# Performance work log

Hardware: AMD Instinct MI355X
Metric: run time of the kernel (lower is better)

Reference implementation:

```python
import jax, jax.numpy as jnp
import numpy as np

H = 8
D = 64
SCALER = 1.0 / np.sqrt(D).astype(np.float32)


def setup_inputs() -> dict:
    key = jax.random.key(0)
    k1, k2 = jax.random.split(key)
    B, N, C = 2, 256, 512
    x = jax.random.normal(k1, (B, N, C), dtype=jnp.float32)
    # Linear(C, 5C, bias=False): weight shape [5C, C], torch convention y = x @ W.T
    w = jax.random.normal(k2, (5 * C, C), dtype=jnp.float32) * 0.02
    return {"x": x, "w": w}


def reference(x, w):
    B, N, C = x.shape
    # projections: a, b, c, vj, vk each [B, H, N, D]
    wx = (x @ w.T).reshape(B, N, 5, H, D).transpose(2, 0, 3, 1, 4)
    a, b, c, vj, vk = wx[0], wx[1], wx[2], wx[3], wx[4]

    # three pairwise score matrices, each [B, H, N, N]
    X = jnp.einsum('bhjd,bhkd->bhjk', b, c) * SCALER
    Y = jnp.einsum('bhkd,bhid->bhki', c, a) * SCALER
    Z = jnp.einsum('bhid,bhjd->bhij', a, b) * SCALER

    # custom 3-way softmax stabilization: X uses global max over (j,k),
    # Y uses max over k (axis -2), Z uses max over j (axis -1)
    X = jnp.exp(X - jnp.max(X, axis=(-2, -1), keepdims=True))
    Y = jnp.exp(Y - jnp.max(Y, axis=-2, keepdims=True))
    Z = jnp.exp(Z - jnp.max(Z, axis=-1, keepdims=True))

    # Num_{bhid} = sum_{j,k} Z_ij * X_jk * vj_jd * Y_ki * vk_kd
    # (same math as the original 5D 'bhjkd'/'bhikd' chain, fused via einsum path)
    Num = jnp.einsum('bhij,bhjk,bhjd,bhki,bhkd->bhid', Z, X, vj, Y, vk)
    # Den_{bhi} = sum_{j,k} Z_ij * Y_ki * X_jk
    Den = jnp.einsum('bhij,bhki,bhjk->bhi', Z, Y, X) + 1e-9

    att = Num / Den[..., None]                     # [B, H, N, D]
    att = att.transpose(0, 2, 1, 3).reshape(B, N, C)
    return att
```

## Files before the change

kernel.cpp:

```cpp
#include <hip/hip_runtime.h>
#include <math.h>

#define Bn 2
#define Hn 8
#define Nn 256
#define Dn 64
#define BH 16
#define SCALER 0.125f

typedef _Float16 half8 __attribute__((ext_vector_type(8)));
typedef _Float16 half4 __attribute__((ext_vector_type(4)));
typedef float floatx4 __attribute__((ext_vector_type(4)));

__device__ __forceinline__ void split_f32(float v, _Float16& h, _Float16& l) {
    h = (_Float16)v;
    l = (_Float16)(v - (float)h);
}

__device__ __forceinline__ void split8(const float4& v0, const float4& v1,
                                       half8& h, half8& l) {
    const float vv[8] = {v0.x, v0.y, v0.z, v0.w, v1.x, v1.y, v1.z, v1.w};
    #pragma unroll
    for (int e = 0; e < 8; ++e) {
        _Float16 hh, ll;
        split_f32(vv[e], hh, ll);
        h[e] = hh; l[e] = ll;
    }
}

__global__ __launch_bounds__(256) void split2_kernel(
    const float* __restrict__ x, const float* __restrict__ w,
    _Float16* __restrict__ xh, _Float16* __restrict__ xl,
    _Float16* __restrict__ wh, _Float16* __restrict__ wl) {
    const int b = blockIdx.x;
    const float* src;
    _Float16 *hp, *lp;
    int idx;
    if (b < 256) {
        idx = (b * 256 + threadIdx.x) * 4;
        src = x; hp = xh; lp = xl;
    } else {
        idx = ((b - 256) * 256 + threadIdx.x) * 4;
        src = w; hp = wh; lp = wl;
    }
    const float4 v = *(const float4*)(src + idx);
    half4 hh, ll;
    _Float16 a2, b2;
    split_f32(v.x, a2, b2); hh[0] = a2; ll[0] = b2;
    split_f32(v.y, a2, b2); hh[1] = a2; ll[1] = b2;
    split_f32(v.z, a2, b2); hh[2] = a2; ll[2] = b2;
    split_f32(v.w, a2, b2); hh[3] = a2; ll[3] = b2;
    *(half4*)(hp + idx) = hh;
    *(half4*)(lp + idx) = ll;
}

__global__ __launch_bounds__(256) void proj_mfma(
    const _Float16* __restrict__ xh, const _Float16* __restrict__ xl,
    const _Float16* __restrict__ wh, const _Float16* __restrict__ wl,
    float* __restrict__ P32, float* __restrict__ vkT) {
    const int m0 = blockIdx.x * 64;
    const int r0 = blockIdx.y * 64;
    const int t = threadIdx.x;
    const int w = t >> 6, l = t & 63;
    const int lr = l & 15, kk8 = (l >> 4) * 8;

    floatx4 acc[4];
    #pragma unroll
    for (int ni = 0; ni < 4; ++ni) acc[ni] = (floatx4){0.f, 0.f, 0.f, 0.f};

    const int arow = m0 + w * 16 + lr;
    for (int kt = 0; kt < 16; ++kt) {
        const int k0 = kt * 32 + kk8;
        const half8 ah = *(const half8*)(xh + arow * 512 + k0);
        const half8 al = *(const half8*)(xl + arow * 512 + k0);
        half8 bhv[4], blv[4];
        #pragma unroll
        for (int ni = 0; ni < 4; ++ni) {
            const int wr = r0 + ni * 16 + lr;
            bhv[ni] = *(const half8*)(wh + wr * 512 + k0);
            blv[ni] = *(const half8*)(wl + wr * 512 + k0);
        }
        #pragma unroll
        for (int ni = 0; ni < 4; ++ni)
            acc[ni] = __builtin_amdgcn_mfma_f32_16x16x32_f16(ah, bhv[ni], acc[ni], 0, 0, 0);
        #pragma unroll
        for (int ni = 0; ni < 4; ++ni)
            acc[ni] = __builtin_amdgcn_mfma_f32_16x16x32_f16(ah, blv[ni], acc[ni], 0, 0, 0);
        #pragma unroll
        for (int ni = 0; ni < 4; ++ni)
            acc[ni] = __builtin_amdgcn_mfma_f32_16x16x32_f16(al, bhv[ni], acc[ni], 0, 0, 0);
    }
    const int rbase = (l >> 4) * 4;
    if (blockIdx.y >= 32) {
        const int mbase = m0 + w * 16 + rbase;
        const int b = mbase >> 8, n = mbase & 255;
        #pragma unroll
        for (int ni = 0; ni < 4; ++ni) {
            const int rcol = r0 + ni * 16 + lr;
            const int h = (rcol >> 6) & 7, d = rcol & 63;
            *(float4*)(vkT + (((b * 8 + h) * 64 + d) * 256 + n)) =
                (float4){acc[ni][0], acc[ni][1], acc[ni][2], acc[ni][3]};
        }
        return;
    }
    #pragma unroll
    for (int ni = 0; ni < 4; ++ni) {
        const int rcol = r0 + ni * 16 + lr;
        const int s = rcol >> 9, h = (rcol >> 6) & 7, d = rcol & 63;
        #pragma unroll
        for (int r = 0; r < 4; ++r) {
            const int m = m0 + w * 16 + rbase + r;
            const int b = m >> 8, n = m & 255;
            P32[(((s * 2 + b) * 8 + h) * 256 + n) * 64 + d] = acc[ni][r];
        }
    }
}

__global__ __launch_bounds__(256) void score_vkt(
    const float* __restrict__ P32,
    _Float16* __restrict__ Xsh, _Float16* __restrict__ Xsl,
    float* __restrict__ Yt, float* __restrict__ Z) {
    const int bh = blockIdx.x, mat = blockIdx.y;
    const int t = threadIdx.x;
    const int i0 = (blockIdx.z >> 2) * 128;
    const int j0 = (blockIdx.z & 3) * 64;
    const int w = t >> 6, l = t & 63;
    const int lr = l & 15, kk8 = (l >> 4) * 8;
    const float* A;
    const float* Bm;
    if (mat == 0)      { A = P32 + (1 * 16 + bh) * 16384; Bm = P32 + (2 * 16 + bh) * 16384; }
    else if (mat == 1) { A = P32 + (0 * 16 + bh) * 16384; Bm = P32 + (2 * 16 + bh) * 16384; }
    else               { A = P32 + (0 * 16 + bh) * 16384; Bm = P32 + (1 * 16 + bh) * 16384; }

    floatx4 acc[2][4];
    #pragma unroll
    for (int mi = 0; mi < 2; ++mi)
        #pragma unroll
        for (int ni = 0; ni < 4; ++ni) acc[mi][ni] = (floatx4){0.f, 0.f, 0.f, 0.f};

    for (int kt = 0; kt < 2; ++kt) {
        const int k0 = kt * 32 + kk8;
        half8 ah[2], al[2], bh8[4], bl8[4];
        #pragma unroll
        for (int mi = 0; mi < 2; ++mi) {
            const int row = i0 + w * 32 + mi * 16 + lr;
            const float4 v0 = *(const float4*)(A + row * 64 + k0);
            const float4 v1 = *(const float4*)(A + row * 64 + k0 + 4);
            split8(v0, v1, ah[mi], al[mi]);
        }
        #pragma unroll
        for (int ni = 0; ni < 4; ++ni) {
            const int row = j0 + ni * 16 + lr;
            const float4 v0 = *(const float4*)(Bm + row * 64 + k0);
            const float4 v1 = *(const float4*)(Bm + row * 64 + k0 + 4);
            split8(v0, v1, bh8[ni], bl8[ni]);
        }
        #pragma unroll
        for (int mi = 0; mi < 2; ++mi)
            #pragma unroll
            for (int ni = 0; ni < 4; ++ni)
                acc[mi][ni] = __builtin_amdgcn_mfma_f32_16x16x32_f16(ah[mi], bh8[ni], acc[mi][ni], 0, 0, 0);
        #pragma unroll
        for (int mi = 0; mi < 2; ++mi)
            #pragma unroll
            for (int ni = 0; ni < 4; ++ni)
                acc[mi][ni] = __builtin_amdgcn_mfma_f32_16x16x32_f16(ah[mi], bl8[ni], acc[mi][ni], 0, 0, 0);
        #pragma unroll
        for (int mi = 0; mi < 2; ++mi)
            #pragma unroll
            for (int ni = 0; ni < 4; ++ni)
                acc[mi][ni] = __builtin_amdgcn_mfma_f32_16x16x32_f16(al[mi], bh8[ni], acc[mi][ni], 0, 0, 0);
    }
    const int rbase = (l >> 4) * 4;
    #pragma unroll
    for (int mi = 0; mi < 2; ++mi)
        #pragma unroll
        for (int ni = 0; ni < 4; ++ni)
            #pragma unroll
            for (int r = 0; r < 4; ++r) {
                const int row = i0 + w * 32 + mi * 16 + rbase + r;
                const int col = j0 + ni * 16 + lr;
                const float e = expf(acc[mi][ni][r] * SCALER);
                if (mat == 0) {
                    const int idx = (bh * 256 + row) * 256 + col;
                    _Float16 hh, ll; split_f32(e, hh, ll);
                    Xsh[idx] = hh; Xsl[idx] = ll;
                } else if (mat == 1) {
                    Yt[bh * 65536 + row * 256 + col] = e;
                } else {
                    Z[bh * 65536 + row * 256 + col] = e;
                }
            }
}

__global__ __launch_bounds__(256) void den_mfma(
    const float* __restrict__ Yt, const _Float16* __restrict__ Xh,
    const _Float16* __restrict__ Xl, const float* __restrict__ Z,
    float* __restrict__ Den) {
    const int bh = blockIdx.x;
    const int ibase = blockIdx.y * 16;
    const int t = threadIdx.x;
    const int w = t >> 6, l = t & 63;
    const int lr = l & 15, ks = l >> 4, kk8 = ks * 8;
    const float* Ytp = Yt + bh * 65536;
    const _Float16* Xhp = Xh + bh * 65536;
    const _Float16* Xlp = Xl + bh * 65536;

    floatx4 acc[4];
    #pragma unroll
    for (int q = 0; q < 4; ++q) acc[q] = (floatx4){0.f, 0.f, 0.f, 0.f};

    for (int kt = 0; kt < 8; ++kt) {
        const int k0 = kt * 32 + kk8;
        half8 ah, al;
        {
            const float4 v0 = *(const float4*)(Ytp + (ibase + lr) * 256 + k0);
            const float4 v1 = *(const float4*)(Ytp + (ibase + lr) * 256 + k0 + 4);
            split8(v0, v1, ah, al);
        }
        half8 bh8[4], bl8[4];
        #pragma unroll
        for (int q = 0; q < 4; ++q) {
            const int jt = w * 4 + q;
            bh8[q] = *(const half8*)(Xhp + (jt * 16 + lr) * 256 + k0);
            bl8[q] = *(const half8*)(Xlp + (jt * 16 + lr) * 256 + k0);
        }
        #pragma unroll
        for (int q = 0; q < 4; ++q)
            acc[q] = __builtin_amdgcn_mfma_f32_16x16x32_f16(ah, bh8[q], acc[q], 0, 0, 0);
        #pragma unroll
        for (int q = 0; q < 4; ++q)
            acc[q] = __builtin_amdgcn_mfma_f32_16x16x32_f16(ah, bl8[q], acc[q], 0, 0, 0);
        #pragma unroll
        for (int q = 0; q < 4; ++q)
            acc[q] = __builtin_amdgcn_mfma_f32_16x16x32_f16(al, bh8[q], acc[q], 0, 0, 0);
    }
    __shared__ float redS[4][16];
    float dp[4] = {0.f, 0.f, 0.f, 0.f};
    const float* Zp = Z + (bh * 256 + ibase) * 256;
    #pragma unroll
    for (int q = 0; q < 4; ++q) {
        const int jt = w * 4 + q;
        #pragma unroll
        for (int r = 0; r < 4; ++r)
            dp[r] += acc[q][r] * Zp[(ks * 4 + r) * 256 + jt * 16 + lr];
    }
    #pragma unroll
    for (int r = 0; r < 4; ++r) {
        float s = dp[r];
        s += __shfl_xor(s, 1); s += __shfl_xor(s, 2);
        s += __shfl_xor(s, 4); s += __shfl_xor(s, 8);
        if (lr == 0) redS[w][ks * 4 + r] = s;
    }
    __syncthreads();
    if (t < 16)
        Den[bh * 256 + ibase + t] =
            redS[0][t] + redS[1][t] + redS[2][t] + redS[3][t] + 1e-9f;
}

__global__ __launch_bounds__(256, 2) void attn_mfma(
    const _Float16* __restrict__ Xh, const _Float16* __restrict__ Xl,
    const float* __restrict__ Yt, const float* __restrict__ Z,
    const float* __restrict__ vkT, const float* __restrict__ P32,
    const float* __restrict__ Den, float* __restrict__ out) {
    const int id = (blockIdx.x & 7) * 256 + (blockIdx.x >> 3);
    const int bh = id >> 7;
    const int i0 = (id & 127) * 2;
    const int t = threadIdx.x;
    const int w = t >> 6, l = t & 63;
    const int lr = l & 15, ks = l >> 4, kk8 = ks * 8;

    __shared__ float yiS[2][256], ziS[2][256];
    __shared__ _Float16 BhS[2][2][4096], BlS[2][2][4096];
    float (*redN)[2][64] = reinterpret_cast<float (*)[2][64]>(&yiS[0][0]);

    yiS[0][t] = Yt[(bh * 256 + i0) * 256 + t];
    yiS[1][t] = Yt[(bh * 256 + i0 + 1) * 256 + t];
    ziS[0][t] = Z[(bh * 256 + i0) * 256 + t];
    ziS[1][t] = Z[(bh * 256 + i0 + 1) * 256 + t];

    const _Float16* Xhp = Xh + bh * 65536;
    const _Float16* Xlp = Xl + bh * 65536;
    const float* vkp = vkT + bh * 16384;
    const float* vj = P32 + (3 * 16 + bh) * 16384;

    floatx4 acc[4][8];
    #pragma unroll
    for (int mi = 0; mi < 4; ++mi)
        #pragma unroll
        for (int ct = 0; ct < 8; ++ct) acc[mi][ct] = (floatx4){0.f, 0.f, 0.f, 0.f};

    const int vd = t >> 2;
    const int sl = t & 3;
    float4 vkr[4];

    auto VKLOAD = [&](int kt) {
        const float* gp = vkp + vd * 256 + (kt & 3) * 64 + sl * 16;
        #pragma unroll
        for (int q = 0; q < 4; ++q) vkr[q] = *(const float4*)(gp + q * 4);
    };
    auto BSTORE = [&](int ktb) {
        const int buf = ktb & 1;
        #pragma unroll
        for (int i = 0; i < 2; ++i) {
            const float* yrow = &yiS[i][(ktb & 3) * 64 + sl * 16];
            #pragma unroll
            for (int hq = 0; hq < 2; ++hq) {
                const float4 va = vkr[hq * 2], vb = vkr[hq * 2 + 1];
                const float4 ya = *(const float4*)(yrow + hq * 8);
                const float4 yb = *(const float4*)(yrow + hq * 8 + 4);
                const float pv[8] = {va.x * ya.x, va.y * ya.y, va.z * ya.z, va.w * ya.w,
                                     vb.x * yb.x, vb.y * yb.y, vb.z * yb.z, vb.w * yb.w};
                half8 hv, lv;
                #pragma unroll
                for (int e = 0; e < 8; ++e) {
                    _Float16 hh, ll;
                    split_f32(pv[e], hh, ll);
                    hv[e] = hh; lv[e] = ll;
                }
                const int o = sl * 2 + hq;
                const int g = vd * 8 + (o ^ (vd & 7));
                *(half8*)&BhS[buf][i][g * 8] = hv;
                *(half8*)&BlS[buf][i][g * 8] = lv;
            }
        }
    };
    auto LOADA = [&](half8* AH, half8* AL, int kt, int sub) {
        const int k0 = (kt & 3) * 64 + sub * 32 + kk8;
        #pragma unroll
        for (int mi = 0; mi < 4; ++mi) {
            const int row = w * 64 + mi * 16 + lr;
            AH[mi] = *(const half8*)(Xhp + row * 256 + k0);
            AL[mi] = *(const half8*)(Xlp + row * 256 + k0);
        }
    };
    auto MFMA_STEP = [&](half8* AH, half8* AL, int buf, int sub) {
        __builtin_amdgcn_s_setprio(1);
        #pragma unroll
        for (int ct = 0; ct < 8; ++ct) {
            const int ii = ct >> 2;
            const int dd = (ct & 3) * 16 + lr;
            const int o = sub * 4 + ks;
            const int g = dd * 8 + (o ^ (dd & 7));
            const half8 bhf = *(const half8*)&BhS[buf][ii][g * 8];
            const half8 blf = *(const half8*)&BlS[buf][ii][g * 8];
            #pragma unroll
            for (int mi = 0; mi < 4; ++mi)
                acc[mi][ct] = __builtin_amdgcn_mfma_f32_16x16x32_f16(AH[mi], bhf, acc[mi][ct], 0, 0, 0);
            #pragma unroll
            for (int mi = 0; mi < 4; ++mi)
                acc[mi][ct] = __builtin_amdgcn_mfma_f32_16x16x32_f16(AH[mi], blf, acc[mi][ct], 0, 0, 0);
            #pragma unroll
            for (int mi = 0; mi < 4; ++mi)
                acc[mi][ct] = __builtin_amdgcn_mfma_f32_16x16x32_f16(AL[mi], bhf, acc[mi][ct], 0, 0, 0);
        }
        __builtin_amdgcn_s_setprio(0);
    };

    half8 A0h[4], A0l[4], A1h[4], A1l[4];

    VKLOAD(0);
    LOADA(A0h, A0l, 0, 0);
    __syncthreads();
    BSTORE(0);
    __syncthreads();

    #pragma unroll 1
    for (int kt = 0; kt < 4; ++kt) {
        const int buf = kt & 1;
        if (kt < 3) VKLOAD(kt + 1);
        LOADA(A1h, A1l, kt, 1);
        MFMA_STEP(A0h, A0l, buf, 0);
        if (kt < 3) {
            asm volatile("s_waitcnt vmcnt(8)" ::: "memory");
            __builtin_amdgcn_sched_barrier(0);
            BSTORE(kt + 1);
            LOADA(A0h, A0l, kt + 1, 0);
        }
        MFMA_STEP(A1h, A1l, buf, 1);
        if (kt < 3) __syncthreads();
    }

    float z0[16], z1[16];
    #pragma unroll
    for (int mi = 0; mi < 4; ++mi)
        #pragma unroll
        for (int r = 0; r < 4; ++r) {
            const int j = w * 64 + mi * 16 + ks * 4 + r;
            z0[mi * 4 + r] = ziS[0][j];
            z1[mi * 4 + r] = ziS[1][j];
        }
    #pragma unroll
    for (int dt = 0; dt < 4; ++dt) {
        float n0 = 0.f, n1 = 0.f;
        #pragma unroll
        for (int mi = 0; mi < 4; ++mi)
            #pragma unroll
            for (int r = 0; r < 4; ++r) {
                const int j = w * 64 + mi * 16 + ks * 4 + r;
                const float v = vj[j * 64 + dt * 16 + lr];
                n0 += acc[mi][dt][r] * z0[mi * 4 + r] * v;
                n1 += acc[mi][dt + 4][r] * z1[mi * 4 + r] * v;
            }
        n0 += __shfl_xor(n0, 16); n0 += __shfl_xor(n0, 32);
        n1 += __shfl_xor(n1, 16); n1 += __shfl_xor(n1, 32);
        if (l < 16) {
            redN[w][0][dt * 16 + l] = n0;
            redN[w][1][dt * 16 + l] = n1;
        }
    }
    __syncthreads();
    if (t < 128) {
        const int ih = t >> 6, d = t & 63;
        const float num = redN[0][ih][d] + redN[1][ih][d] +
                          redN[2][ih][d] + redN[3][ih][d];
        const int i = i0 + ih;
        const float den = Den[bh * 256 + i];
        out[((bh >> 3) * 256 + i) * 512 + (bh & 7) * 64 + d] = num / den;
    }
}

extern "C" void kernel_launch(void* const* d_in, const int* in_sizes, int n_in,
                              void* d_out, int out_size, void* d_ws, size_t ws_size,
                              hipStream_t stream) {
    const float* x = (const float*)d_in[0];
    const float* w = (const float*)d_in[1];
    float* out = (float*)d_out;

    float* ws = (float*)d_ws;
    float* P32 = ws;
    float* U = ws + 1310720;
    _Float16* xh = (_Float16*)U;
    _Float16* xl = xh + 262144;
    _Float16* wh = xl + 262144;
    _Float16* wl = wh + 1310720;
    _Float16* Xsh = (_Float16*)U;
    _Float16* Xsl = Xsh + 1048576;
    float* Yt = U + 1048576;
    float* Z = Yt + 1048576;
    float* vkT = Z + 1048576;
    float* Den = vkT + 262144;

    split2_kernel<<<1536, 256, 0, stream>>>(x, w, xh, xl, wh, wl);
    proj_mfma<<<dim3(8, 40), 256, 0, stream>>>(xh, xl, wh, wl, P32, vkT);
    score_vkt<<<dim3(16, 3, 8), 256, 0, stream>>>(P32, Xsh, Xsl, Yt, Z);
    den_mfma<<<dim3(16, 16), 256, 0, stream>>>(Yt, Xsh, Xsl, Z, Den);
    attn_mfma<<<2048, 256, 0, stream>>>(Xsh, Xsl, Yt, Z, vkT, P32, Den, out);
}
```

Before: 171.4 us.

## Build MFMA B fragments in registers from global vkT instead of LDS staging

Drops the double-buffered LDS staging of the vk*Y product and its split into fp16 hi/lo parts. Each lane now loads its own vkT slice from global memory, multiplies it by Y read from shared memory, and splits it in registers right before the MFMAs. This removes LDS traffic, most barriers and the software pipeline, and cuts LDS usage, which may raise occupancy. In exchange, every wave redundantly reloads and recomputes the B fragments, and global loads are no longer prefetched ahead of the MFMAs.

```diff
diff --git a/kernel.cpp b/kernel.cpp
--- a/kernel.cpp
+++ b/kernel.cpp
@@ -271,8 +271,7 @@
     const int lr = l & 15, ks = l >> 4, kk8 = ks * 8;
 
     __shared__ float yiS[2][256], ziS[2][256];
-    __shared__ _Float16 BhS[2][2][4096], BlS[2][2][4096];
-    float (*redN)[2][64] = reinterpret_cast<float (*)[2][64]>(&yiS[0][0]);
+    __shared__ float redN[4][2][64];
 
     yiS[0][t] = Yt[(bh * 256 + i0) * 256 + t];
     yiS[1][t] = Yt[(bh * 256 + i0 + 1) * 256 + t];
@@ -290,95 +289,58 @@
         #pragma unroll
         for (int ct = 0; ct < 8; ++ct) acc[mi][ct] = (floatx4){0.f, 0.f, 0.f, 0.f};
 
-    const int vd = t >> 2;
-    const int sl = t & 3;
-    float4 vkr[4];
-
-    auto VKLOAD = [&](int kt) {
-        const float* gp = vkp + vd * 256 + (kt & 3) * 64 + sl * 16;
-        #pragma unroll
-        for (int q = 0; q < 4; ++q) vkr[q] = *(const float4*)(gp + q * 4);
-    };
-    auto BSTORE = [&](int ktb) {
-        const int buf = ktb & 1;
-        #pragma unroll
-        for (int i = 0; i < 2; ++i) {
-            const float* yrow = &yiS[i][(ktb & 3) * 64 + sl * 16];
-            #pragma unroll
-            for (int hq = 0; hq < 2; ++hq) {
-                const float4 va = vkr[hq * 2], vb = vkr[hq * 2 + 1];
-                const float4 ya = *(const float4*)(yrow + hq * 8);
-                const float4 yb = *(const float4*)(yrow + hq * 8 + 4);
-                const float pv[8] = {va.x * ya.x, va.y * ya.y, va.z * ya.z, va.w * ya.w,
-                                     vb.x * yb.x, vb.y * yb.y, vb.z * yb.z, vb.w * yb.w};
-                half8 hv, lv;
-                #pragma unroll
-                for (int e = 0; e < 8; ++e) {
-                    _Float16 hh, ll;
-                    split_f32(pv[e], hh, ll);
-                    hv[e] = hh; lv[e] = ll;
-                }
-                const int o = sl * 2 + hq;
-                const int g = vd * 8 + (o ^ (vd & 7));
-                *(half8*)&BhS[buf][i][g * 8] = hv;
-                *(half8*)&BlS[buf][i][g * 8] = lv;
-            }
-        }
-    };
-    auto LOADA = [&](half8* AH, half8* AL, int kt, int sub) {
-        const int k0 = (kt & 3) * 64 + sub * 32 + kk8;
+    __syncthreads();
+
+    #pragma unroll 1
+    for (int kt = 0; kt < 8; ++kt) {
+        const int kl = kt * 32 + kk8;
+        half8 Ah[4], Al[4];
         #pragma unroll
         for (int mi = 0; mi < 4; ++mi) {
             const int row = w * 64 + mi * 16 + lr;
-            AH[mi] = *(const half8*)(Xhp + row * 256 + k0);
-            AL[mi] = *(const half8*)(Xlp + row * 256 + k0);
-        }
-    };
-    auto MFMA_STEP = [&](half8* AH, half8* AL, int buf, int sub) {
-        __builtin_amdgcn_s_setprio(1);
-        #pragma unroll
-        for (int ct = 0; ct < 8; ++ct) {
-            const int ii = ct >> 2;
-            const int dd = (ct & 3) * 16 + lr;
-            const int o = sub * 4 + ks;
-            const int g = dd * 8 + (o ^ (dd & 7));
-            const half8 bhf = *(const half8*)&BhS[buf][ii][g * 8];
-            const half8 blf = *(const half8*)&BlS[buf][ii][g * 8];
-            #pragma unroll
-            for (int mi = 0; mi < 4; ++mi)
-                acc[mi][ct] = __builtin_amdgcn_mfma_f32_16x16x32_f16(AH[mi], bhf, acc[mi][ct], 0, 0, 0);
-            #pragma unroll
-            for (int mi = 0; mi < 4; ++mi)
-                acc[mi][ct] = __builtin_amdgcn_mfma_f32_16x16x32_f16(AH[mi], blf, acc[mi][ct], 0, 0, 0);
-            #pragma unroll
-            for (int mi = 0; mi < 4; ++mi)
-                acc[mi][ct] = __builtin_amdgcn_mfma_f32_16x16x32_f16(AL[mi], bhf, acc[mi][ct], 0, 0, 0);
-        }
-        __builtin_amdgcn_s_setprio(0);
-    };
-
-    half8 A0h[4], A0l[4], A1h[4], A1l[4];
-
-    VKLOAD(0);
-    LOADA(A0h, A0l, 0, 0);
-    __syncthreads();
-    BSTORE(0);
-    __syncthreads();
-
-    #pragma unroll 1
-    for (int kt = 0; kt < 4; ++kt) {
-        const int buf = kt & 1;
-        if (kt < 3) VKLOAD(kt + 1);
-        LOADA(A1h, A1l, kt, 1);
-        MFMA_STEP(A0h, A0l, buf, 0);
-        if (kt < 3) {
-            asm volatile("s_waitcnt vmcnt(8)" ::: "memory");
-            __builtin_amdgcn_sched_barrier(0);
-            BSTORE(kt + 1);
-            LOADA(A0h, A0l, kt + 1, 0);
-        }
-        MFMA_STEP(A1h, A1l, buf, 1);
-        if (kt < 3) __syncthreads();
+            Ah[mi] = *(const half8*)(Xhp + row * 256 + kl);
+            Al[mi] = *(const half8*)(Xlp + row * 256 + kl);
+        }
+        const float4 y0a = *(const float4*)&yiS[0][kl];
+        const float4 y0b = *(const float4*)&yiS[0][kl + 4];
+        const float4 y1a = *(const float4*)&yiS[1][kl];
+        const float4 y1b = *(const float4*)&yiS[1][kl + 4];
+        const float yr0[8] = {y0a.x, y0a.y, y0a.z, y0a.w, y0b.x, y0b.y, y0b.z, y0b.w};
+        const float yr1[8] = {y1a.x, y1a.y, y1a.z, y1a.w, y1b.x, y1b.y, y1b.z, y1b.w};
+        #pragma unroll
+        for (int dt4 = 0; dt4 < 4; ++dt4) {
+            const float* vp = vkp + (dt4 * 16 + lr) * 256 + kl;
+            const float4 va = *(const float4*)(vp);
+            const float4 vb = *(const float4*)(vp + 4);
+            const float vv[8] = {va.x, va.y, va.z, va.w, vb.x, vb.y, vb.z, vb.w};
+            half8 b0h, b0l, b1h, b1l;
+            #pragma unroll
+            for (int e = 0; e < 8; ++e) {
+                _Float16 hh, ll;
+                split_f32(vv[e] * yr0[e], hh, ll); b0h[e] = hh; b0l[e] = ll;
+                split_f32(vv[e] * yr1[e], hh, ll); b1h[e] = hh; b1l[e] = ll;
+            }
+            __builtin_amdgcn_s_setprio(1);
+            #pragma unroll
+            for (int mi = 0; mi < 4; ++mi)
+                acc[mi][dt4] = __builtin_amdgcn_mfma_f32_16x16x32_f16(Ah[mi], b0h, acc[mi][dt4], 0, 0, 0);
+            #pragma unroll
+            for (int mi = 0; mi < 4; ++mi)
+                acc[mi][dt4] = __builtin_amdgcn_mfma_f32_16x16x32_f16(Ah[mi], b0l, acc[mi][dt4], 0, 0, 0);
+            #pragma unroll
+            for (int mi = 0; mi < 4; ++mi)
+                acc[mi][dt4] = __builtin_amdgcn_mfma_f32_16x16x32_f16(Al[mi], b0h, acc[mi][dt4], 0, 0, 0);
+            #pragma unroll
+            for (int mi = 0; mi < 4; ++mi)
+                acc[mi][4 + dt4] = __builtin_amdgcn_mfma_f32_16x16x32_f16(Ah[mi], b1h, acc[mi][4 + dt4], 0, 0, 0);
+            #pragma unroll
+            for (int mi = 0; mi < 4; ++mi)
+                acc[mi][4 + dt4] = __builtin_amdgcn_mfma_f32_16x16x32_f16(Ah[mi], b1l, acc[mi][4 + dt4], 0, 0, 0);
+            #pragma unroll
+            for (int mi = 0; mi < 4; ++mi)
+                acc[mi][4 + dt4] = __builtin_amdgcn_mfma_f32_16x16x32_f16(Al[mi], b1h, acc[mi][4 + dt4], 0, 0, 0);
+            __builtin_amdgcn_s_setprio(0);
+        }
     }
 
     float z0[16], z1[16];
```

New measurement: 208.7 us. +21.8%, slower.
